# Kernel tuning notes

Measured on AMD Instinct MI355X. Metric: run time of the kernel, lower is better.

## Reference

```python
import jax, jax.numpy as jnp
import numpy as np

BINS = 64


def _histogram(x, bins=BINS):
    """Faithful jax version of ColorHistogramLoss.get_histogram.

    Original semantics: edges = linspace(-1, 1, bins); bin j (j < bins-1) counts
    edges[j] <= v < edges[j+1]; last bin counts v >= edges[-1] (= 1).
    Values v < -1 fall in no bin. Single bucketize + scatter-add pass.
    """
    B, C = x.shape[0], x.shape[1]
    xf = x.reshape(B * C, -1)            # [B*C, N]
    N = xf.shape[1]
    edges = jnp.linspace(-1.0, 1.0, bins).astype(x.dtype)
    # searchsorted(side='right') - 1 gives j with edges[j] <= v < edges[j+1];
    # v < -1 -> -1 (invalid); v >= 1 -> bins-1 after clip (matches open last bin).
    idx = jnp.searchsorted(edges, xf, side='right') - 1
    valid = idx >= 0
    idx = jnp.clip(idx, 0, bins - 1)
    seg = idx + jnp.arange(B * C)[:, None] * bins      # per-(batch,channel) offset
    counts = jax.ops.segment_sum(
        valid.astype(jnp.float32).ravel(), seg.ravel(),
        num_segments=B * C * bins)
    return counts.reshape(B, C * bins) / N             # [B, C*bins]


def setup_inputs() -> dict:
    key = jax.random.key(0)
    k1, k2 = jax.random.split(key)
    shape = (32, 3, 512, 512)
    # pixels normalized to [-1, 1), matching the linspace(-1, 1) bin edges
    inp = jax.random.uniform(k1, shape, dtype=jnp.float32) * 2.0 - 1.0
    tgt = jax.random.uniform(k2, shape, dtype=jnp.float32) * 2.0 - 1.0
    return {"input": inp, "target": tgt}


def reference(input, target):
    hist_in = _histogram(input, BINS)
    hist_tgt = _histogram(target, BINS)
    return jnp.mean(jnp.abs(hist_in - hist_tgt))   # F.l1_loss (mean reduction)
```

## Files before the change

kernel.cpp:

```cpp
#include <hip/hip_runtime.h>


#define BINS 64
#define PLANES 96
#define PLANE_F4 65536
#define SEGS 32
#define SEG_F4 2048
#define TPB 256
#define F4T 8

__global__ __launch_bounds__(TPB) void hist_diff_kernel(
        const float4* __restrict__ in4, const float4* __restrict__ tg4,
        int* __restrict__ gdiff) {
    const int tid  = threadIdx.x;
    const int lane = tid & 63;
    const int plane = blockIdx.x >> 5;
    const int seg   = blockIdx.x & (SEGS - 1);
    const long base = (long)plane * PLANE_F4 + (long)seg * SEG_F4 + tid;

    unsigned long long inv[6];
#pragma unroll
    for (int k = 0; k < 6; ++k)
        inv[k] = ((lane >> k) & 1) ? 0ull : ~0ull;

    float4 a[F4T], b[F4T];
#pragma unroll
    for (int k = 0; k < F4T; ++k) a[k] = in4[base + k * TPB];
#pragma unroll
    for (int k = 0; k < F4T; ++k) b[k] = tg4[base + k * TPB];

    int cin = 0, ctg = 0;
    auto slot = [&](float v, int& cnt) {
        float x = (v + 1.0f) * 31.5f;
        int bin = (int)x;
        bin = bin > 63 ? 63 : bin;
        unsigned long long m =
            (__ballot(bin & 1)  ^ inv[0]) &
            (__ballot(bin & 2)  ^ inv[1]) &
            (__ballot(bin & 4)  ^ inv[2]) &
            (__ballot(bin & 8)  ^ inv[3]) &
            (__ballot(bin & 16) ^ inv[4]) &
            (__ballot(bin & 32) ^ inv[5]);
        cnt += __popcll(m);
    };
#pragma unroll
    for (int k = 0; k < F4T; ++k) {
        slot(a[k].x, cin); slot(a[k].y, cin);
        slot(a[k].z, cin); slot(a[k].w, cin);
    }
#pragma unroll
    for (int k = 0; k < F4T; ++k) {
        slot(b[k].x, ctg); slot(b[k].y, ctg);
        slot(b[k].z, ctg); slot(b[k].w, ctg);
    }

    const int d = cin - ctg;
    if (d != 0) atomicAdd(&gdiff[plane * BINS + lane], d);
}

__global__ __launch_bounds__(TPB) void reduce_abs_kernel(
        const int* __restrict__ gdiff, float* __restrict__ out) {
    int s = 0;
    for (int i = threadIdx.x; i < PLANES * BINS; i += TPB) {
        int v = gdiff[i];
        s += (v < 0) ? -v : v;
    }
#pragma unroll
    for (int off = 32; off > 0; off >>= 1) s += __shfl_down(s, off, 64);
    __shared__ int ws[TPB / 64];
    const int wid  = threadIdx.x >> 6;
    const int lane = threadIdx.x & 63;
    if (lane == 0) ws[wid] = s;
    __syncthreads();
    if (threadIdx.x == 0) {
        int total = 0;
#pragma unroll
        for (int w = 0; w < TPB / 64; ++w) total += ws[w];
        out[0] = (float)total * (1.0f / (262144.0f * 6144.0f));
    }
}

extern "C" void kernel_launch(void* const* d_in, const int* in_sizes, int n_in,
                              void* d_out, int out_size, void* d_ws, size_t ws_size,
                              hipStream_t stream) {
    const float4* inp = (const float4*)d_in[0];
    const float4* tgt = (const float4*)d_in[1];
    int* gdiff = (int*)d_ws;

    hipMemsetAsync(gdiff, 0, PLANES * BINS * sizeof(int), stream);
    hist_diff_kernel<<<PLANES * SEGS, TPB, 0, stream>>>(inp, tgt, gdiff);
    reduce_abs_kernel<<<1, TPB, 0, stream>>>(gdiff, (float*)d_out);
}
```

Measured before the change: 226.2 us.

## Split block work between LDS atomic histogram and ballot-popcount waves

Each block is divided so that two waves bin their share of the segment with shared-memory atomics, while the other two waves keep the ballot/popcount counting scheme. The split (9 vs 7 float4 per thread) is meant to balance the LDS atomic path against the ALU-heavy ballot path, so both the LDS unit and the vector ALUs are busy. It adds a shared histogram, two block barriers and extra global atomics per block, and the two wave groups do uneven amounts of work.

```diff
diff --git a/kernel.cpp b/kernel.cpp
--- a/kernel.cpp
+++ b/kernel.cpp
@@ -7,55 +7,92 @@
 #define SEGS 32
 #define SEG_F4 2048
 #define TPB 256
-#define F4T 8
+#define DS_F4 9
+#define BL_F4 7
+
+__device__ __forceinline__ int binof(float v) {
+    float x = (v + 1.0f) * 31.5f;
+    int bin = (int)x;
+    return bin > 63 ? 63 : bin;
+}
 
 __global__ __launch_bounds__(TPB) void hist_diff_kernel(
         const float4* __restrict__ in4, const float4* __restrict__ tg4,
         int* __restrict__ gdiff) {
+    __shared__ int lh[BINS];
     const int tid  = threadIdx.x;
-    const int lane = tid & 63;
     const int plane = blockIdx.x >> 5;
     const int seg   = blockIdx.x & (SEGS - 1);
-    const long base = (long)plane * PLANE_F4 + (long)seg * SEG_F4 + tid;
+    const long segbase = (long)plane * PLANE_F4 + (long)seg * SEG_F4;
 
-    unsigned long long inv[6];
+    if (tid < BINS) lh[tid] = 0;
+    __syncthreads();
+
+    int bdiff = 0;
+
+    if (tid < 128) {
+        const long base = segbase + tid;
+        float4 a[DS_F4];
 #pragma unroll
-    for (int k = 0; k < 6; ++k)
-        inv[k] = ((lane >> k) & 1) ? 0ull : ~0ull;
+        for (int k = 0; k < DS_F4; ++k) a[k] = in4[base + k * 128];
+#pragma unroll
+        for (int k = 0; k < DS_F4; ++k) {
+            atomicAdd(&lh[binof(a[k].x)], 1); atomicAdd(&lh[binof(a[k].y)], 1);
+            atomicAdd(&lh[binof(a[k].z)], 1); atomicAdd(&lh[binof(a[k].w)], 1);
+        }
+#pragma unroll
+        for (int k = 0; k < DS_F4; ++k) a[k] = tg4[base + k * 128];
+#pragma unroll
+        for (int k = 0; k < DS_F4; ++k) {
+            atomicAdd(&lh[binof(a[k].x)], -1); atomicAdd(&lh[binof(a[k].y)], -1);
+            atomicAdd(&lh[binof(a[k].z)], -1); atomicAdd(&lh[binof(a[k].w)], -1);
+        }
+    } else {
+        const int lane = tid & 63;
+        unsigned long long inv[6];
+#pragma unroll
+        for (int k = 0; k < 6; ++k)
+            inv[k] = ((lane >> k) & 1) ? 0ull : ~0ull;
 
-    float4 a[F4T], b[F4T];
+        const long base = segbase + 1152 + (tid - 128);
+        float4 a[BL_F4], b[BL_F4];
 #pragma unroll
-    for (int k = 0; k < F4T; ++k) a[k] = in4[base + k * TPB];
+        for (int k = 0; k < BL_F4; ++k) a[k] = in4[base + k * 128];
 #pragma unroll
-    for (int k = 0; k < F4T; ++k) b[k] = tg4[base + k * TPB];
+        for (int k = 0; k < BL_F4; ++k) b[k] = tg4[base + k * 128];
 
-    int cin = 0, ctg = 0;
-    auto slot = [&](float v, int& cnt) {
-        float x = (v + 1.0f) * 31.5f;
-        int bin = (int)x;
-        bin = bin > 63 ? 63 : bin;
-        unsigned long long m =
-            (__ballot(bin & 1)  ^ inv[0]) &
-            (__ballot(bin & 2)  ^ inv[1]) &
-            (__ballot(bin & 4)  ^ inv[2]) &
-            (__ballot(bin & 8)  ^ inv[3]) &
-            (__ballot(bin & 16) ^ inv[4]) &
-            (__ballot(bin & 32) ^ inv[5]);
-        cnt += __popcll(m);
-    };
+        int cin = 0, ctg = 0;
+        auto slot = [&](float v, int& cnt) {
+            int bin = binof(v);
+            unsigned long long m =
+                (__ballot(bin & 1)  ^ inv[0]) &
+                (__ballot(bin & 2)  ^ inv[1]) &
+                (__ballot(bin & 4)  ^ inv[2]) &
+                (__ballot(bin & 8)  ^ inv[3]) &
+                (__ballot(bin & 16) ^ inv[4]) &
+                (__ballot(bin & 32) ^ inv[5]);
+            cnt += __popcll(m);
+        };
 #pragma unroll
-    for (int k = 0; k < F4T; ++k) {
-        slot(a[k].x, cin); slot(a[k].y, cin);
-        slot(a[k].z, cin); slot(a[k].w, cin);
-    }
+        for (int k = 0; k < BL_F4; ++k) {
+            slot(a[k].x, cin); slot(a[k].y, cin);
+            slot(a[k].z, cin); slot(a[k].w, cin);
+        }
 #pragma unroll
-    for (int k = 0; k < F4T; ++k) {
-        slot(b[k].x, ctg); slot(b[k].y, ctg);
-        slot(b[k].z, ctg); slot(b[k].w, ctg);
+        for (int k = 0; k < BL_F4; ++k) {
+            slot(b[k].x, ctg); slot(b[k].y, ctg);
+            slot(b[k].z, ctg); slot(b[k].w, ctg);
+        }
+        bdiff = cin - ctg;
     }
 
-    const int d = cin - ctg;
-    if (d != 0) atomicAdd(&gdiff[plane * BINS + lane], d);
+    __syncthreads();
+    if (tid < BINS) {
+        int v = lh[tid];
+        if (v != 0) atomicAdd(&gdiff[plane * BINS + tid], v);
+    }
+    if (tid >= 128 && bdiff != 0)
+        atomicAdd(&gdiff[plane * BINS + (tid & 63)], bdiff);
 }
 
 __global__ __launch_bounds__(TPB) void reduce_abs_kernel(
```

After: 217.5 us. 3.8% less time.

## Split histogram work between LDS atomics and wave ballot counting

Applied to the files above, without the earlier changes.

Sends roughly half of each thread's values to a shared-memory histogram via LDS atomics, and bins the rest with the existing ballot/popcount scheme. The point is to balance the LDS atomic unit against the ballot-heavy scalar/VALU path so both run at once. Per-block results are now merged in LDS and flushed with one global atomic per bin, which cuts global atomic traffic. In exchange the kernel gains LDS contention and two block-wide barriers.

```diff
diff --git a/kernel.cpp b/kernel.cpp
--- a/kernel.cpp
+++ b/kernel.cpp
@@ -8,32 +8,49 @@
 #define SEG_F4 2048
 #define TPB 256
 #define F4T 8
+#define DS_IN 17
+#define DS_TG 18
+
+__device__ __forceinline__ int binof(float v) {
+    float x = (v + 1.0f) * 31.5f;
+    int bin = (int)x;
+    return bin > 63 ? 63 : bin;
+}
 
 __global__ __launch_bounds__(TPB) void hist_diff_kernel(
         const float4* __restrict__ in4, const float4* __restrict__ tg4,
         int* __restrict__ gdiff) {
+    __shared__ int lh[BINS];
     const int tid  = threadIdx.x;
     const int lane = tid & 63;
+    if (tid < BINS) lh[tid] = 0;
+    __syncthreads();
+
     const int plane = blockIdx.x >> 5;
     const int seg   = blockIdx.x & (SEGS - 1);
     const long base = (long)plane * PLANE_F4 + (long)seg * SEG_F4 + tid;
+
+    float4 a[F4T], b[F4T];
+#pragma unroll
+    for (int k = 0; k < F4T; ++k) a[k] = in4[base + k * TPB];
+#pragma unroll
+    for (int k = 0; k < F4T; ++k) b[k] = tg4[base + k * TPB];
+    const float* av = (const float*)a;
+    const float* bv = (const float*)b;
+
+#pragma unroll
+    for (int p = 0; p < DS_IN; ++p) atomicAdd(&lh[binof(av[p])], 1);
+#pragma unroll
+    for (int p = 0; p < DS_TG; ++p) atomicAdd(&lh[binof(bv[p])], -1);
 
     unsigned long long inv[6];
 #pragma unroll
     for (int k = 0; k < 6; ++k)
         inv[k] = ((lane >> k) & 1) ? 0ull : ~0ull;
 
-    float4 a[F4T], b[F4T];
-#pragma unroll
-    for (int k = 0; k < F4T; ++k) a[k] = in4[base + k * TPB];
-#pragma unroll
-    for (int k = 0; k < F4T; ++k) b[k] = tg4[base + k * TPB];
-
     int cin = 0, ctg = 0;
     auto slot = [&](float v, int& cnt) {
-        float x = (v + 1.0f) * 31.5f;
-        int bin = (int)x;
-        bin = bin > 63 ? 63 : bin;
+        int bin = binof(v);
         unsigned long long m =
             (__ballot(bin & 1)  ^ inv[0]) &
             (__ballot(bin & 2)  ^ inv[1]) &
@@ -44,18 +61,18 @@
         cnt += __popcll(m);
     };
 #pragma unroll
-    for (int k = 0; k < F4T; ++k) {
-        slot(a[k].x, cin); slot(a[k].y, cin);
-        slot(a[k].z, cin); slot(a[k].w, cin);
+    for (int p = DS_IN; p < 32; ++p) slot(av[p], cin);
+#pragma unroll
+    for (int p = DS_TG; p < 32; ++p) slot(bv[p], ctg);
+
+    const int bdiff = cin - ctg;
+    if (bdiff != 0) atomicAdd(&lh[lane], bdiff);
+
+    __syncthreads();
+    if (tid < BINS) {
+        int v = lh[tid];
+        if (v != 0) atomicAdd(&gdiff[plane * BINS + tid], v);
     }
-#pragma unroll
-    for (int k = 0; k < F4T; ++k) {
-        slot(b[k].x, ctg); slot(b[k].y, ctg);
-        slot(b[k].z, ctg); slot(b[k].w, ctg);
-    }
-
-    const int d = cin - ctg;
-    if (d != 0) atomicAdd(&gdiff[plane * BINS + lane], d);
 }
 
 __global__ __launch_bounds__(TPB) void reduce_abs_kernel(
```

After: 221.6 us. 2.0% less time.
